# Performance work log

Hardware: AMD Instinct MI355X
Metric: run time of the kernel (lower is better)

The kernel has to match this reference:

```python
import jax, jax.numpy as jnp
import numpy as np

B, T, C = 2, 2048, 2048
N_HEAD, N_KV_HEAD = 16, 4
HEAD_DIM = C // N_HEAD  # 128
HALF = HEAD_DIM // 2    # 64


def _rms_norm(x):
    # F.rms_norm with no weight: x / sqrt(mean(x^2) + eps), eps = dtype eps
    eps = jnp.finfo(x.dtype).eps
    return x * jax.lax.rsqrt(jnp.mean(x * x, axis=-1, keepdims=True) + eps)


def _rope_apply(x, cos, sin):
    # x: [B, H, T, Hs]; cos/sin: [1, 1, T, Hs/2]
    x1, x2 = x[..., :HALF], x[..., HALF:]
    return jnp.concatenate([x1 * cos - x2 * sin, x1 * sin + x2 * cos], axis=-1)


def setup_inputs() -> dict:
    key = jax.random.key(0)
    ks = jax.random.split(key, 8)
    x = jax.random.normal(ks[0], (B, T, C), dtype=jnp.float32)
    # real RoPE tables (base 10000), shape [1,1,T,HALF]
    inv_freq = 1.0 / (10000.0 ** (np.arange(0, HALF, dtype=np.float32) / HALF))
    t = np.arange(T, dtype=np.float32)
    ang = np.einsum('t,f->tf', t, inv_freq)
    cos = jnp.asarray(np.cos(ang))[None, None]
    sin = jnp.asarray(np.sin(ang))[None, None]
    s = 0.02
    Wq = jax.random.normal(ks[1], (C, N_HEAD * HEAD_DIM), dtype=jnp.float32) * s
    Wk = jax.random.normal(ks[2], (C, N_KV_HEAD * HEAD_DIM), dtype=jnp.float32) * s
    Wv = jax.random.normal(ks[3], (C, N_KV_HEAD * HEAD_DIM), dtype=jnp.float32) * s
    Wo = jax.random.normal(ks[4], (C, C), dtype=jnp.float32) * s
    bo = jnp.zeros((C,), dtype=jnp.float32)
    return {"x": x, "cos": cos, "sin": sin, "Wq": Wq, "Wk": Wk, "Wv": Wv, "Wo": Wo, "bo": bo}


def reference(x, cos, sin, Wq, Wk, Wv, Wo, bo):
    Bq, Tq, Cq = x.shape
    G = N_HEAD // N_KV_HEAD
    # QKV projections (GQA, no bias)
    q = (x @ Wq).reshape(Bq, Tq, N_HEAD, HEAD_DIM)
    k = (x @ Wk).reshape(Bq, Tq, N_KV_HEAD, HEAD_DIM)
    v = (x @ Wv).reshape(Bq, Tq, N_KV_HEAD, HEAD_DIM)
    # QK RMSNorm (over head_dim), then to [B, H, T, Hs]
    q = jnp.transpose(_rms_norm(q), (0, 2, 1, 3))
    k = jnp.transpose(_rms_norm(k), (0, 2, 1, 3))
    v = jnp.transpose(v, (0, 2, 1, 3))
    # RoPE
    q = _rope_apply(q, cos[:, :, :Tq, :], sin[:, :, :Tq, :])
    k = _rope_apply(k, cos[:, :, :Tq, :], sin[:, :, :Tq, :])
    # GQA: repeat kv heads across groups
    k = jnp.repeat(k, G, axis=1)  # [B, H, T, Hs]
    v = jnp.repeat(v, G, axis=1)
    # Causal SDPA
    scale = 1.0 / jnp.sqrt(jnp.asarray(HEAD_DIM, dtype=x.dtype))
    scores = jnp.einsum('bhqd,bhkd->bhqk', q, k) * scale
    causal = jnp.tril(jnp.ones((Tq, Tq), dtype=bool))
    scores = jnp.where(causal, scores, jnp.asarray(-jnp.inf, dtype=scores.dtype))
    attn = jax.nn.softmax(scores, axis=-1)
    y = jnp.einsum('bhqk,bhkd->bhqd', attn, v)
    y = jnp.transpose(y, (0, 2, 1, 3)).reshape(Bq, Tq, Cq)
    return y @ Wo + bo
```

## Files before the change

kernel.cpp:

```cpp
#include <hip/hip_runtime.h>
#include <hip/hip_bf16.h>
#include <math.h>

#define BB 2
#define TT 2048
#define CC 2048
#define NH 16
#define NKV 4
#define HD 128
#define HALF 64
#define MTOT (BB*TT)
#define NQKV (CC + 2*NKV*HD)

typedef unsigned short u16;
typedef __attribute__((ext_vector_type(8))) short bf16x8;
typedef __attribute__((ext_vector_type(4))) float f32x4;

__device__ __forceinline__ u16 f2bf(float f) {
  unsigned u = __float_as_uint(f);
  unsigned r = (u + 0x7FFFu + ((u >> 16) & 1u)) >> 16;
  return (u16)r;
}

__device__ __forceinline__ void gl_lds16(const void* g, void* l) {
  __builtin_amdgcn_global_load_lds(
      (const __attribute__((address_space(1))) unsigned int*)g,
      (__attribute__((address_space(3))) unsigned int*)l, 16, 0, 0);
}

__global__ __launch_bounds__(256) void convert_bf16(
    const float* __restrict__ src, u16* __restrict__ dst, int n8) {
  int i = blockIdx.x * 256 + threadIdx.x;
  if (i >= n8) return;
  const float4* s4 = (const float4*)src;
  float4 a = s4[(size_t)i * 2], b = s4[(size_t)i * 2 + 1];
  bf16x8 o;
  o[0] = (short)f2bf(a.x); o[1] = (short)f2bf(a.y);
  o[2] = (short)f2bf(a.z); o[3] = (short)f2bf(a.w);
  o[4] = (short)f2bf(b.x); o[5] = (short)f2bf(b.y);
  o[6] = (short)f2bf(b.z); o[7] = (short)f2bf(b.w);
  ((bf16x8*)dst)[i] = o;
}

__global__ __launch_bounds__(256) void transpose_w(
    const float* __restrict__ W, u16* __restrict__ Wt, int N, int row_off) {
  __shared__ float tile[32][33];
  const int n0 = blockIdx.x * 32, k0 = blockIdx.y * 32;
  const int tx = threadIdx.x, ty = threadIdx.y;
#pragma unroll
  for (int i = 0; i < 4; ++i)
    tile[ty + 8 * i][tx] = W[(size_t)(k0 + ty + 8 * i) * N + n0 + tx];
  __syncthreads();
#pragma unroll
  for (int i = 0; i < 4; ++i)
    Wt[(size_t)(row_off + n0 + ty + 8 * i) * CC + k0 + tx] =
        f2bf(tile[tx][ty + 8 * i]);
}

__global__ __launch_bounds__(256) void v_transpose(
    const float* __restrict__ qkv_lin, u16* __restrict__ vt) {
  __shared__ float tile[32][33];
  const int t0 = blockIdx.x * 32, d0 = blockIdx.y * 32;
  const int p = blockIdx.z;
  const int b = p >> 2, kv = p & 3;
  const int tx = threadIdx.x, ty = threadIdx.y;
#pragma unroll
  for (int i = 0; i < 4; ++i)
    tile[ty + 8 * i][tx] =
        qkv_lin[(size_t)(b * TT + t0 + ty + 8 * i) * NQKV + CC + NKV * HD + kv * HD + d0 + tx];
  __syncthreads();
#pragma unroll
  for (int i = 0; i < 4; ++i)
    vt[((size_t)p * HD + d0 + ty + 8 * i) * TT + t0 + tx] =
        f2bf(tile[tx][ty + 8 * i]);
}

__global__ __launch_bounds__(256) void gemm_bt_bf16(
    const u16* __restrict__ A, const u16* __restrict__ Bt,
    const float* __restrict__ bias, float* __restrict__ C,
    int M, int N, int K) {
  __shared__ u16 As[128 * 32];
  __shared__ u16 Bs[128 * 32];
  const int tid = threadIdx.x;
  const int wave = tid >> 6, lane = tid & 63;
  const int quad = lane >> 4, lo = lane & 15;
  const int bm = blockIdx.y * 128, bn = blockIdx.x * 128;
  const int wm = (wave & 1) * 64, wn = (wave >> 1) * 64;

  f32x4 acc[4][4];
#pragma unroll
  for (int i = 0; i < 4; ++i)
#pragma unroll
    for (int j = 0; j < 4; ++j)
#pragma unroll
      for (int r = 0; r < 4; ++r) acc[i][j][r] = 0.f;

  const int iss0 = wave * 2, iss1 = wave * 2 + 1;
  const int e0 = iss0 * 512 + lane * 8, e1 = iss1 * 512 + lane * 8;
  const int r0 = e0 >> 5, c0 = e0 & 31;
  const int r1 = e1 >> 5, c1 = e1 & 31;

  for (int k0 = 0; k0 < K; k0 += 32) {
    gl_lds16(A + (size_t)(bm + r0) * K + k0 + c0, (char*)As + iss0 * 1024);
    gl_lds16(A + (size_t)(bm + r1) * K + k0 + c1, (char*)As + iss1 * 1024);
    gl_lds16(Bt + (size_t)(bn + r0) * K + k0 + c0, (char*)Bs + iss0 * 1024);
    gl_lds16(Bt + (size_t)(bn + r1) * K + k0 + c1, (char*)Bs + iss1 * 1024);
    __syncthreads();

    bf16x8 af[4], bg[4];
#pragma unroll
    for (int i = 0; i < 4; ++i)
      af[i] = *(const bf16x8*)&As[(wm + i * 16 + lo) * 32 + quad * 8];
#pragma unroll
    for (int j = 0; j < 4; ++j)
      bg[j] = *(const bf16x8*)&Bs[(wn + j * 16 + lo) * 32 + quad * 8];
#pragma unroll
    for (int i = 0; i < 4; ++i)
#pragma unroll
      for (int j = 0; j < 4; ++j)
        acc[i][j] = __builtin_amdgcn_mfma_f32_16x16x32_bf16(af[i], bg[j], acc[i][j], 0, 0, 0);
    __syncthreads();
  }

#pragma unroll
  for (int i = 0; i < 4; ++i)
#pragma unroll
    for (int j = 0; j < 4; ++j)
#pragma unroll
      for (int r = 0; r < 4; ++r) {
        int row = bm + wm + i * 16 + quad * 4 + r;
        int col = bn + wn + j * 16 + lo;
        float v = acc[i][j][r];
        if (bias) v += bias[col];
        C[(size_t)row * N + col] = v;
      }
}

__global__ __launch_bounds__(256) void qkv_post(
    const float* __restrict__ qkv_lin, const float* __restrict__ cosp,
    const float* __restrict__ sinp, u16* __restrict__ q, u16* __restrict__ k) {
  const int bt = blockIdx.x;
  const int hh = blockIdx.y * 4 + (threadIdx.x >> 6);
  const int lane = threadIdx.x & 63;
  const int t = bt & (TT - 1), b = bt >> 11;
  const int col = (hh < NH) ? hh * HD : CC + (hh - NH) * HD;
  const float* src = qkv_lin + (size_t)bt * NQKV + col;
  float v1 = src[lane], v2 = src[lane + 64];
  float ss = v1 * v1 + v2 * v2;
#pragma unroll
  for (int mm = 1; mm < 64; mm <<= 1) ss += __shfl_xor(ss, mm, 64);
  float rms = rsqrtf(ss * (1.f / 128.f) + 1.1920929e-7f);
  float c = cosp[t * HALF + lane], s = sinp[t * HALF + lane];
  float o1 = v1 * rms * c - v2 * rms * s;
  float o2 = v1 * rms * s + v2 * rms * c;
  if (hh < NH) {
    u16* dst = q + (((size_t)(b * NH + hh)) * TT + t) * HD;
    dst[lane] = f2bf(o1); dst[lane + 64] = f2bf(o2);
  } else {
    u16* dst = k + (((size_t)(b * NKV + (hh - NH))) * TT + t) * HD;
    dst[lane] = f2bf(o1); dst[lane + 64] = f2bf(o2);
  }
}

__device__ __forceinline__ void softmax_rb(
    const f32x4* sacc, float* l_lane, u16* Pdst, int rowb, int t0,
    int lo, int quad) {
  const float cc = 0.12751744050808612f;
  if (t0 + 63 > rowb) {
#pragma unroll
    for (int ct = 0; ct < 4; ++ct) {
      const int kvc = ct * 16 + lo;
      const int kcol = t0 + kvc;
      const int idx = (kvc >> 5) * 512 + ((kvc >> 3) & 3) * 128 + quad * 32 + (kvc & 7);
#pragma unroll
      for (int r = 0; r < 4; ++r) {
        float e = __builtin_amdgcn_exp2f(sacc[ct][r] * cc);
        if (kcol > rowb + r) e = 0.f;
        l_lane[r] += e;
        Pdst[idx + r * 8] = f2bf(e);
      }
    }
  } else {
#pragma unroll
    for (int ct = 0; ct < 4; ++ct) {
      const int kvc = ct * 16 + lo;
      const int idx = (kvc >> 5) * 512 + ((kvc >> 3) & 3) * 128 + quad * 32 + (kvc & 7);
#pragma unroll
      for (int r = 0; r < 4; ++r) {
        float e = __builtin_amdgcn_exp2f(sacc[ct][r] * cc);
        l_lane[r] += e;
        Pdst[idx + r * 8] = f2bf(e);
      }
    }
  }
}

__global__ __launch_bounds__(256, 2) void attn_mfma(
    const u16* __restrict__ Qb, const u16* __restrict__ Kb,
    const u16* __restrict__ Vt, u16* __restrict__ Y) {
  __shared__ u16 Ks[2][8192];
  __shared__ u16 Vs[8192];
  __shared__ u16 Ps[4][2048];

  const int qt = blockIdx.x;
  const int bh = blockIdx.y;
  const int b = bh >> 4, h = bh & 15, kvh = h >> 2;
  const int tid = threadIdx.x;
  const int wave = tid >> 6, lane = tid & 63;
  const int quad = lane >> 4, lo = lane & 15;

  const int rowsA = qt * 64;
  const int rowsB = (31 - qt) * 64;
  const u16* Qg = Qb + (size_t)(b * NH + h) * TT * HD;
  const u16* Kg = Kb + (size_t)(b * NKV + kvh) * TT * HD;
  const u16* Vg = Vt + (size_t)(b * NKV + kvh) * HD * TT;

  bf16x8 aq[2][4];
#pragma unroll
  for (int kc = 0; kc < 4; ++kc) {
    aq[0][kc] = *(const bf16x8*)(Qg + (size_t)(rowsA + wave * 16 + lo) * HD + kc * 32 + quad * 8);
    aq[1][kc] = *(const bf16x8*)(Qg + (size_t)(rowsB + wave * 16 + lo) * HD + kc * 32 + quad * 8);
  }

  const u16* kgp[4]; const u16* vgp[4];
  u16* klp[2][4]; u16* vlp[4];
#pragma unroll
  for (int c = 0; c < 4; ++c) {
    const int s = wave * 4 + c;
    const int ct = s >> 2, kq = s & 3;
    kgp[c] = Kg + (size_t)(ct * 16 + lo) * HD + kq * 32 + quad * 8;
    const int dt = s >> 1, k2 = s & 1;
    vgp[c] = Vg + (size_t)(dt * 16 + lo) * TT + k2 * 32 + quad * 8;
    klp[0][c] = &Ks[0][s * 512]; klp[1][c] = &Ks[1][s * 512];
    vlp[c] = &Vs[s * 512];
  }

  f32x4 oacc[2][8];
#pragma unroll
  for (int rb = 0; rb < 2; ++rb)
#pragma unroll
    for (int dt = 0; dt < 8; ++dt)
#pragma unroll
      for (int r = 0; r < 4; ++r) oacc[rb][dt][r] = 0.f;
  float l_lane[2][4];
#pragma unroll
  for (int rb = 0; rb < 2; ++rb)
#pragma unroll
    for (int r = 0; r < 4; ++r) l_lane[rb][r] = 0.f;

  u16* Pw = Ps[wave];
  const int ntiles = 32 - qt;

#pragma unroll
  for (int c = 0; c < 4; ++c) { gl_lds16(kgp[c], klp[0][c]); kgp[c] += 64 * HD; }

  for (int nt = 0; nt < ntiles; ++nt) {
    const int par = nt & 1;
    __syncthreads();
#pragma unroll
    for (int c = 0; c < 4; ++c) { gl_lds16(vgp[c], vlp[c]); vgp[c] += 64; }
    if (nt + 1 < ntiles) {
#pragma unroll
      for (int c = 0; c < 4; ++c) { gl_lds16(kgp[c], klp[par ^ 1][c]); kgp[c] += 64 * HD; }
    }
    const u16* ksb = Ks[par];
    const int t0 = nt * 64;
    const bool act0 = (nt <= qt);

    f32x4 sacc[2][4];
#pragma unroll
    for (int rb = 0; rb < 2; ++rb)
#pragma unroll
      for (int ct = 0; ct < 4; ++ct)
#pragma unroll
        for (int r = 0; r < 4; ++r) sacc[rb][ct][r] = 0.f;
    if (act0) {
#pragma unroll
      for (int ct = 0; ct < 4; ++ct)
#pragma unroll
        for (int kc = 0; kc < 4; ++kc) {
          bf16x8 bk = *(const bf16x8*)&ksb[(ct * 4 + kc) * 512 + lane * 8];
          sacc[0][ct] = __builtin_amdgcn_mfma_f32_16x16x32_bf16(aq[0][kc], bk, sacc[0][ct], 0, 0, 0);
          sacc[1][ct] = __builtin_amdgcn_mfma_f32_16x16x32_bf16(aq[1][kc], bk, sacc[1][ct], 0, 0, 0);
        }
    } else {
#pragma unroll
      for (int ct = 0; ct < 4; ++ct)
#pragma unroll
        for (int kc = 0; kc < 4; ++kc) {
          bf16x8 bk = *(const bf16x8*)&ksb[(ct * 4 + kc) * 512 + lane * 8];
          sacc[1][ct] = __builtin_amdgcn_mfma_f32_16x16x32_bf16(aq[1][kc], bk, sacc[1][ct], 0, 0, 0);
        }
    }

    softmax_rb(sacc[1], l_lane[1], Pw + 1024,
               rowsB + wave * 16 + quad * 4, t0, lo, quad);
    if (act0)
      softmax_rb(sacc[0], l_lane[0], Pw,
                 rowsA + wave * 16 + quad * 4, t0, lo, quad);

    __syncthreads();

    if (act0) {
      bf16x8 ap0[2], ap1[2];
#pragma unroll
      for (int k2 = 0; k2 < 2; ++k2) {
        ap0[k2] = *(const bf16x8*)&Pw[k2 * 512 + lane * 8];
        ap1[k2] = *(const bf16x8*)&Pw[(2 + k2) * 512 + lane * 8];
      }
#pragma unroll
      for (int dt = 0; dt < 8; ++dt)
#pragma unroll
        for (int k2 = 0; k2 < 2; ++k2) {
          bf16x8 bv = *(const bf16x8*)&Vs[(dt * 2 + k2) * 512 + lane * 8];
          oacc[0][dt] = __builtin_amdgcn_mfma_f32_16x16x32_bf16(ap0[k2], bv, oacc[0][dt], 0, 0, 0);
          oacc[1][dt] = __builtin_amdgcn_mfma_f32_16x16x32_bf16(ap1[k2], bv, oacc[1][dt], 0, 0, 0);
        }
    } else {
      bf16x8 ap1[2];
#pragma unroll
      for (int k2 = 0; k2 < 2; ++k2)
        ap1[k2] = *(const bf16x8*)&Pw[(2 + k2) * 512 + lane * 8];
#pragma unroll
      for (int dt = 0; dt < 8; ++dt)
#pragma unroll
        for (int k2 = 0; k2 < 2; ++k2) {
          bf16x8 bv = *(const bf16x8*)&Vs[(dt * 2 + k2) * 512 + lane * 8];
          oacc[1][dt] = __builtin_amdgcn_mfma_f32_16x16x32_bf16(ap1[k2], bv, oacc[1][dt], 0, 0, 0);
        }
    }
  }

#pragma unroll
  for (int rb = 0; rb < 2; ++rb)
#pragma unroll
    for (int r = 0; r < 4; ++r) {
      float l = l_lane[rb][r];
#pragma unroll
      for (int mm = 1; mm < 16; mm <<= 1) l += __shfl_xor(l, mm, 64);
      l_lane[rb][r] = 1.f / l;
    }
#pragma unroll
  for (int rb = 0; rb < 2; ++rb) {
    const int rows = (rb == 0) ? rowsA : rowsB;
    const size_t row0 = (size_t)b * TT + rows + wave * 16 + quad * 4;
#pragma unroll
    for (int dt = 0; dt < 8; ++dt)
#pragma unroll
      for (int r = 0; r < 4; ++r)
        Y[(row0 + r) * CC + h * HD + dt * 16 + lo] = f2bf(oacc[rb][dt][r] * l_lane[rb][r]);
  }
}

extern "C" void kernel_launch(void* const* d_in, const int* in_sizes, int n_in,
                              void* d_out, int out_size, void* d_ws, size_t ws_size,
                              hipStream_t stream) {
  (void)in_sizes; (void)n_in; (void)out_size; (void)ws_size;
  const float* x    = (const float*)d_in[0];
  const float* cosp = (const float*)d_in[1];
  const float* sinp = (const float*)d_in[2];
  const float* Wq   = (const float*)d_in[3];
  const float* Wk   = (const float*)d_in[4];
  const float* Wv   = (const float*)d_in[5];
  const float* Wo   = (const float*)d_in[6];
  const float* bo   = (const float*)d_in[7];
  float* out = (float*)d_out;
  char* ws = (char*)d_ws;

  const size_t MB = 1024 * 1024;
  u16*   xb      = (u16*)(ws);
  u16*   Wt      = (u16*)(ws + 16 * MB);
  float* qkv_lin = (float*)(ws + 28 * MB);
  u16*   Wot     = (u16*)(ws + 76 * MB);
  u16*   qb_buf  = (u16*)(ws);
  u16*   kb      = (u16*)(ws + 16 * MB);
  u16*   vt      = (u16*)(ws + 20 * MB);
  u16*   y       = (u16*)(ws + 28 * MB);

  convert_bf16<<<(MTOT * CC / 8 + 255) / 256, 256, 0, stream>>>(x, xb, MTOT * CC / 8);

  transpose_w<<<dim3(CC / 32, CC / 32), dim3(32, 8), 0, stream>>>(Wq, Wt, CC, 0);
  transpose_w<<<dim3(NKV * HD / 32, CC / 32), dim3(32, 8), 0, stream>>>(Wk, Wt, NKV * HD, CC);
  transpose_w<<<dim3(NKV * HD / 32, CC / 32), dim3(32, 8), 0, stream>>>(Wv, Wt, NKV * HD, CC + NKV * HD);
  transpose_w<<<dim3(CC / 32, CC / 32), dim3(32, 8), 0, stream>>>(Wo, Wot, CC, 0);

  gemm_bt_bf16<<<dim3(NQKV / 128, MTOT / 128), 256, 0, stream>>>(
      xb, Wt, nullptr, qkv_lin, MTOT, NQKV, CC);

  qkv_post<<<dim3(MTOT, 5), 256, 0, stream>>>(qkv_lin, cosp, sinp, qb_buf, kb);

  v_transpose<<<dim3(TT / 32, HD / 32, BB * NKV), dim3(32, 8), 0, stream>>>(qkv_lin, vt);

  attn_mfma<<<dim3(16, BB * NH), 256, 0, stream>>>(qb_buf, kb, vt, y);

  gemm_bt_bf16<<<dim3(CC / 128, MTOT / 128), 256, 0, stream>>>(
      y, Wot, bo, out, MTOT, CC, CC);
}
```

Measured before the change: 345.4 us.

## Fuse prep kernels, emit bf16 QKV, keep attention P in registers

Merges the x conversion and the four weight transposes into one launch. The QKV GEMM now writes bf16 instead of fp32, which halves that intermediate's traffic for qkv_post and v_transpose. In attention, S is computed transposed so the softmax probabilities can be packed straight into MFMA operand registers. This removes the P round-trip through LDS and one barrier per tile, and V is double-buffered with its prefetch moved alongside K. V's transpose is permuted to match the new register layout, and the extra bf16 rounding of the QKV intermediate adds a small precision cost.

```diff
diff --git a/kernel.cpp b/kernel.cpp
--- a/kernel.cpp
+++ b/kernel.cpp
@@ -21,6 +21,9 @@
   unsigned r = (u + 0x7FFFu + ((u >> 16) & 1u)) >> 16;
   return (u16)r;
 }
+__device__ __forceinline__ float bf2f(u16 v) {
+  return __uint_as_float(((unsigned)v) << 16);
+}
 
 __device__ __forceinline__ void gl_lds16(const void* g, void* l) {
   __builtin_amdgcn_global_load_lds(
@@ -28,57 +31,48 @@
       (__attribute__((address_space(3))) unsigned int*)l, 16, 0, 0);
 }
 
-__global__ __launch_bounds__(256) void convert_bf16(
-    const float* __restrict__ src, u16* __restrict__ dst, int n8) {
-  int i = blockIdx.x * 256 + threadIdx.x;
-  if (i >= n8) return;
-  const float4* s4 = (const float4*)src;
-  float4 a = s4[(size_t)i * 2], b = s4[(size_t)i * 2 + 1];
-  bf16x8 o;
-  o[0] = (short)f2bf(a.x); o[1] = (short)f2bf(a.y);
-  o[2] = (short)f2bf(a.z); o[3] = (short)f2bf(a.w);
-  o[4] = (short)f2bf(b.x); o[5] = (short)f2bf(b.y);
-  o[6] = (short)f2bf(b.z); o[7] = (short)f2bf(b.w);
-  ((bf16x8*)dst)[i] = o;
-}
-
-__global__ __launch_bounds__(256) void transpose_w(
-    const float* __restrict__ W, u16* __restrict__ Wt, int N, int row_off) {
+__global__ __launch_bounds__(256) void prep(
+    const float* __restrict__ x, const float* __restrict__ Wq,
+    const float* __restrict__ Wk, const float* __restrict__ Wv,
+    const float* __restrict__ Wo, u16* __restrict__ xb,
+    u16* __restrict__ Wt, u16* __restrict__ Wot) {
+  const int z = blockIdx.z;
+  const int tx = threadIdx.x, ty = threadIdx.y;
+  if (z == 4) {
+    const int tid = ty * 32 + tx;
+    const int i = (blockIdx.y * 64 + blockIdx.x) * 256 + tid;
+    const float4* s4 = (const float4*)x;
+    float4 a = s4[(size_t)i * 2], b = s4[(size_t)i * 2 + 1];
+    bf16x8 o;
+    o[0] = (short)f2bf(a.x); o[1] = (short)f2bf(a.y);
+    o[2] = (short)f2bf(a.z); o[3] = (short)f2bf(a.w);
+    o[4] = (short)f2bf(b.x); o[5] = (short)f2bf(b.y);
+    o[6] = (short)f2bf(b.z); o[7] = (short)f2bf(b.w);
+    ((bf16x8*)xb)[i] = o;
+    return;
+  }
+  const float* W; u16* dst; int N; int row_off;
+  if (z == 0)      { W = Wq; dst = Wt;  N = 2048; row_off = 0; }
+  else if (z == 1) { W = Wk; dst = Wt;  N = 512;  row_off = 2048; }
+  else if (z == 2) { W = Wv; dst = Wt;  N = 512;  row_off = 2560; }
+  else             { W = Wo; dst = Wot; N = 2048; row_off = 0; }
+  const int n0 = blockIdx.x * 32, k0 = blockIdx.y * 32;
+  if (n0 >= N) return;
   __shared__ float tile[32][33];
-  const int n0 = blockIdx.x * 32, k0 = blockIdx.y * 32;
-  const int tx = threadIdx.x, ty = threadIdx.y;
 #pragma unroll
   for (int i = 0; i < 4; ++i)
     tile[ty + 8 * i][tx] = W[(size_t)(k0 + ty + 8 * i) * N + n0 + tx];
   __syncthreads();
 #pragma unroll
   for (int i = 0; i < 4; ++i)
-    Wt[(size_t)(row_off + n0 + ty + 8 * i) * CC + k0 + tx] =
-        f2bf(tile[tx][ty + 8 * i]);
-}
-
-__global__ __launch_bounds__(256) void v_transpose(
-    const float* __restrict__ qkv_lin, u16* __restrict__ vt) {
-  __shared__ float tile[32][33];
-  const int t0 = blockIdx.x * 32, d0 = blockIdx.y * 32;
-  const int p = blockIdx.z;
-  const int b = p >> 2, kv = p & 3;
-  const int tx = threadIdx.x, ty = threadIdx.y;
-#pragma unroll
-  for (int i = 0; i < 4; ++i)
-    tile[ty + 8 * i][tx] =
-        qkv_lin[(size_t)(b * TT + t0 + ty + 8 * i) * NQKV + CC + NKV * HD + kv * HD + d0 + tx];
-  __syncthreads();
-#pragma unroll
-  for (int i = 0; i < 4; ++i)
-    vt[((size_t)p * HD + d0 + ty + 8 * i) * TT + t0 + tx] =
+    dst[(size_t)(row_off + n0 + ty + 8 * i) * CC + k0 + tx] =
         f2bf(tile[tx][ty + 8 * i]);
 }
 
 __global__ __launch_bounds__(256) void gemm_bt_bf16(
     const u16* __restrict__ A, const u16* __restrict__ Bt,
     const float* __restrict__ bias, float* __restrict__ C,
-    int M, int N, int K) {
+    int M, int N, int K, int out_bf16) {
   __shared__ u16 As[128 * 32];
   __shared__ u16 Bs[128 * 32];
   const int tid = threadIdx.x;
@@ -132,20 +126,21 @@
         int col = bn + wn + j * 16 + lo;
         float v = acc[i][j][r];
         if (bias) v += bias[col];
-        C[(size_t)row * N + col] = v;
+        if (out_bf16) ((u16*)C)[(size_t)row * N + col] = f2bf(v);
+        else          C[(size_t)row * N + col] = v;
       }
 }
 
 __global__ __launch_bounds__(256) void qkv_post(
-    const float* __restrict__ qkv_lin, const float* __restrict__ cosp,
+    const u16* __restrict__ qkv_lin, const float* __restrict__ cosp,
     const float* __restrict__ sinp, u16* __restrict__ q, u16* __restrict__ k) {
   const int bt = blockIdx.x;
   const int hh = blockIdx.y * 4 + (threadIdx.x >> 6);
   const int lane = threadIdx.x & 63;
   const int t = bt & (TT - 1), b = bt >> 11;
   const int col = (hh < NH) ? hh * HD : CC + (hh - NH) * HD;
-  const float* src = qkv_lin + (size_t)bt * NQKV + col;
-  float v1 = src[lane], v2 = src[lane + 64];
+  const u16* src = qkv_lin + (size_t)bt * NQKV + col;
+  float v1 = bf2f(src[lane]), v2 = bf2f(src[lane + 64]);
   float ss = v1 * v1 + v2 * v2;
 #pragma unroll
   for (int mm = 1; mm < 64; mm <<= 1) ss += __shfl_xor(ss, mm, 64);
@@ -162,36 +157,54 @@
   }
 }
 
-__device__ __forceinline__ void softmax_rb(
-    const f32x4* sacc, float* l_lane, u16* Pdst, int rowb, int t0,
-    int lo, int quad) {
+__global__ __launch_bounds__(256) void v_transpose(
+    const u16* __restrict__ qkv_lin, u16* __restrict__ vt) {
+  __shared__ u16 tile[32][33];
+  const int t0 = blockIdx.x * 32, d0 = blockIdx.y * 32;
+  const int p = blockIdx.z;
+  const int b = p >> 2, kv = p & 3;
+  const int tx = threadIdx.x, ty = threadIdx.y;
+#pragma unroll
+  for (int i = 0; i < 4; ++i)
+    tile[ty + 8 * i][tx] =
+        qkv_lin[(size_t)(b * TT + t0 + ty + 8 * i) * NQKV + CC + NKV * HD + kv * HD + d0 + tx];
+  __syncthreads();
+  const int tperm = ((tx >> 2) & 3) * 8 + (tx & 3) + 4 * ((tx >> 4) & 1);
+#pragma unroll
+  for (int i = 0; i < 4; ++i)
+    vt[((size_t)p * HD + d0 + ty + 8 * i) * TT + t0 + tperm] = tile[tx][ty + 8 * i];
+}
+
+__device__ __forceinline__ void softmax_pack(
+    const f32x4* sacc, float& l_lane, bf16x8* ap, int rowq, int t0,
+    bool diag, int quad) {
   const float cc = 0.12751744050808612f;
-  if (t0 + 63 > rowb) {
-#pragma unroll
-    for (int ct = 0; ct < 4; ++ct) {
-      const int kvc = ct * 16 + lo;
-      const int kcol = t0 + kvc;
-      const int idx = (kvc >> 5) * 512 + ((kvc >> 3) & 3) * 128 + quad * 32 + (kvc & 7);
+  float e[4][4];
+  if (diag) {
+#pragma unroll
+    for (int ct = 0; ct < 4; ++ct)
 #pragma unroll
       for (int r = 0; r < 4; ++r) {
-        float e = __builtin_amdgcn_exp2f(sacc[ct][r] * cc);
-        if (kcol > rowb + r) e = 0.f;
-        l_lane[r] += e;
-        Pdst[idx + r * 8] = f2bf(e);
-      }
-    }
+        float v = __builtin_amdgcn_exp2f(sacc[ct][r] * cc);
+        if (t0 + ct * 16 + quad * 4 + r > rowq) v = 0.f;
+        l_lane += v; e[ct][r] = v;
+      }
   } else {
 #pragma unroll
-    for (int ct = 0; ct < 4; ++ct) {
-      const int kvc = ct * 16 + lo;
-      const int idx = (kvc >> 5) * 512 + ((kvc >> 3) & 3) * 128 + quad * 32 + (kvc & 7);
+    for (int ct = 0; ct < 4; ++ct)
 #pragma unroll
       for (int r = 0; r < 4; ++r) {
-        float e = __builtin_amdgcn_exp2f(sacc[ct][r] * cc);
-        l_lane[r] += e;
-        Pdst[idx + r * 8] = f2bf(e);
-      }
-    }
+        float v = __builtin_amdgcn_exp2f(sacc[ct][r] * cc);
+        l_lane += v; e[ct][r] = v;
+      }
+  }
+#pragma unroll
+  for (int k2 = 0; k2 < 2; ++k2) {
+    bf16x8 ch;
+#pragma unroll
+    for (int j = 0; j < 8; ++j)
+      ch[j] = (short)f2bf(e[k2 * 2 + (j >> 2)][j & 3]);
+    ap[k2] = ch;
   }
 }
 
@@ -199,8 +212,7 @@
     const u16* __restrict__ Qb, const u16* __restrict__ Kb,
     const u16* __restrict__ Vt, u16* __restrict__ Y) {
   __shared__ u16 Ks[2][8192];
-  __shared__ u16 Vs[8192];
-  __shared__ u16 Ps[4][2048];
+  __shared__ u16 Vs[2][8192];
 
   const int qt = blockIdx.x;
   const int bh = blockIdx.y;
@@ -209,8 +221,7 @@
   const int wave = tid >> 6, lane = tid & 63;
   const int quad = lane >> 4, lo = lane & 15;
 
-  const int rowsA = qt * 64;
-  const int rowsB = (31 - qt) * 64;
+  const int rowsA = qt * 64, rowsB = (31 - qt) * 64;
   const u16* Qg = Qb + (size_t)(b * NH + h) * TT * HD;
   const u16* Kg = Kb + (size_t)(b * NKV + kvh) * TT * HD;
   const u16* Vg = Vt + (size_t)(b * NKV + kvh) * HD * TT;
@@ -223,7 +234,7 @@
   }
 
   const u16* kgp[4]; const u16* vgp[4];
-  u16* klp[2][4]; u16* vlp[4];
+  u16* klp[2][4]; u16* vlp[2][4];
 #pragma unroll
   for (int c = 0; c < 4; ++c) {
     const int s = wave * 4 + c;
@@ -232,7 +243,7 @@
     const int dt = s >> 1, k2 = s & 1;
     vgp[c] = Vg + (size_t)(dt * 16 + lo) * TT + k2 * 32 + quad * 8;
     klp[0][c] = &Ks[0][s * 512]; klp[1][c] = &Ks[1][s * 512];
-    vlp[c] = &Vs[s * 512];
+    vlp[0][c] = &Vs[0][s * 512]; vlp[1][c] = &Vs[1][s * 512];
   }
 
   f32x4 oacc[2][8];
@@ -242,28 +253,30 @@
     for (int dt = 0; dt < 8; ++dt)
 #pragma unroll
       for (int r = 0; r < 4; ++r) oacc[rb][dt][r] = 0.f;
-  float l_lane[2][4];
-#pragma unroll
-  for (int rb = 0; rb < 2; ++rb)
-#pragma unroll
-    for (int r = 0; r < 4; ++r) l_lane[rb][r] = 0.f;
-
-  u16* Pw = Ps[wave];
+  float l_lane[2] = {0.f, 0.f};
+
   const int ntiles = 32 - qt;
-
-#pragma unroll
-  for (int c = 0; c < 4; ++c) { gl_lds16(kgp[c], klp[0][c]); kgp[c] += 64 * HD; }
+  const int rowqA = rowsA + wave * 16 + lo;
+  const int rowqB = rowsB + wave * 16 + lo;
+
+#pragma unroll
+  for (int c = 0; c < 4; ++c) {
+    gl_lds16(kgp[c], klp[0][c]); kgp[c] += 64 * HD;
+    gl_lds16(vgp[c], vlp[0][c]); vgp[c] += 64;
+  }
 
   for (int nt = 0; nt < ntiles; ++nt) {
     const int par = nt & 1;
     __syncthreads();
-#pragma unroll
-    for (int c = 0; c < 4; ++c) { gl_lds16(vgp[c], vlp[c]); vgp[c] += 64; }
     if (nt + 1 < ntiles) {
 #pragma unroll
-      for (int c = 0; c < 4; ++c) { gl_lds16(kgp[c], klp[par ^ 1][c]); kgp[c] += 64 * HD; }
+      for (int c = 0; c < 4; ++c) {
+        gl_lds16(kgp[c], klp[par ^ 1][c]); kgp[c] += 64 * HD;
+        gl_lds16(vgp[c], vlp[par ^ 1][c]); vgp[c] += 64;
+      }
     }
     const u16* ksb = Ks[par];
+    const u16* vsb = Vs[par];
     const int t0 = nt * 64;
     const bool act0 = (nt <= qt);
 
@@ -274,72 +287,45 @@
       for (int ct = 0; ct < 4; ++ct)
 #pragma unroll
         for (int r = 0; r < 4; ++r) sacc[rb][ct][r] = 0.f;
-    if (act0) {
-#pragma unroll
-      for (int ct = 0; ct < 4; ++ct)
-#pragma unroll
-        for (int kc = 0; kc < 4; ++kc) {
-          bf16x8 bk = *(const bf16x8*)&ksb[(ct * 4 + kc) * 512 + lane * 8];
-          sacc[0][ct] = __builtin_amdgcn_mfma_f32_16x16x32_bf16(aq[0][kc], bk, sacc[0][ct], 0, 0, 0);
-          sacc[1][ct] = __builtin_amdgcn_mfma_f32_16x16x32_bf16(aq[1][kc], bk, sacc[1][ct], 0, 0, 0);
-        }
-    } else {
-#pragma unroll
-      for (int ct = 0; ct < 4; ++ct)
-#pragma unroll
-        for (int kc = 0; kc < 4; ++kc) {
-          bf16x8 bk = *(const bf16x8*)&ksb[(ct * 4 + kc) * 512 + lane * 8];
-          sacc[1][ct] = __builtin_amdgcn_mfma_f32_16x16x32_bf16(aq[1][kc], bk, sacc[1][ct], 0, 0, 0);
-        }
-    }
-
-    softmax_rb(sacc[1], l_lane[1], Pw + 1024,
-               rowsB + wave * 16 + quad * 4, t0, lo, quad);
+#pragma unroll
+    for (int ct = 0; ct < 4; ++ct)
+#pragma unroll
+      for (int kc = 0; kc < 4; ++kc) {
+        bf16x8 bk = *(const bf16x8*)&ksb[(ct * 4 + kc) * 512 + lane * 8];
+        sacc[1][ct] = __builtin_amdgcn_mfma_f32_16x16x32_bf16(bk, aq[1][kc], sacc[1][ct], 0, 0, 0);
+        if (act0)
+          sacc[0][ct] = __builtin_amdgcn_mfma_f32_16x16x32_bf16(bk, aq[0][kc], sacc[0][ct], 0, 0, 0);
+      }
+
+    bf16x8 ap[2][2];
+    softmax_pack(sacc[1], l_lane[1], ap[1], rowqB, t0,
+                 t0 + 63 > rowsB + wave * 16, quad);
     if (act0)
-      softmax_rb(sacc[0], l_lane[0], Pw,
-                 rowsA + wave * 16 + quad * 4, t0, lo, quad);
-
-    __syncthreads();
-
-    if (act0) {
-      bf16x8 ap0[2], ap1[2];
+      softmax_pack(sacc[0], l_lane[0], ap[0], rowqA, t0,
+                   t0 + 63 > rowsA + wave * 16, quad);
+
+#pragma unroll
+    for (int dt = 0; dt < 8; ++dt)
 #pragma unroll
       for (int k2 = 0; k2 < 2; ++k2) {
-        ap0[k2] = *(const bf16x8*)&Pw[k2 * 512 + lane * 8];
-        ap1[k2] = *(const bf16x8*)&Pw[(2 + k2) * 512 + lane * 8];
-      }
-#pragma unroll
-      for (int dt = 0; dt < 8; ++dt)
-#pragma unroll
-        for (int k2 = 0; k2 < 2; ++k2) {
-          bf16x8 bv = *(const bf16x8*)&Vs[(dt * 2 + k2) * 512 + lane * 8];
-          oacc[0][dt] = __builtin_amdgcn_mfma_f32_16x16x32_bf16(ap0[k2], bv, oacc[0][dt], 0, 0, 0);
-          oacc[1][dt] = __builtin_amdgcn_mfma_f32_16x16x32_bf16(ap1[k2], bv, oacc[1][dt], 0, 0, 0);
-        }
-    } else {
-      bf16x8 ap1[2];
-#pragma unroll
-      for (int k2 = 0; k2 < 2; ++k2)
-        ap1[k2] = *(const bf16x8*)&Pw[(2 + k2) * 512 + lane * 8];
-#pragma unroll
-      for (int dt = 0; dt < 8; ++dt)
-#pragma unroll
-        for (int k2 = 0; k2 < 2; ++k2) {
-          bf16x8 bv = *(const bf16x8*)&Vs[(dt * 2 + k2) * 512 + lane * 8];
-          oacc[1][dt] = __builtin_amdgcn_mfma_f32_16x16x32_bf16(ap1[k2], bv, oacc[1][dt], 0, 0, 0);
-        }
-    }
-  }
-
-#pragma unroll
-  for (int rb = 0; rb < 2; ++rb)
-#pragma unroll
-    for (int r = 0; r < 4; ++r) {
-      float l = l_lane[rb][r];
-#pragma unroll
-      for (int mm = 1; mm < 16; mm <<= 1) l += __shfl_xor(l, mm, 64);
-      l_lane[rb][r] = 1.f / l;
-    }
+        bf16x8 bv = *(const bf16x8*)&vsb[(dt * 2 + k2) * 512 + lane * 8];
+        oacc[1][dt] = __builtin_amdgcn_mfma_f32_16x16x32_bf16(ap[1][k2], bv, oacc[1][dt], 0, 0, 0);
+        if (act0)
+          oacc[0][dt] = __builtin_amdgcn_mfma_f32_16x16x32_bf16(ap[0][k2], bv, oacc[0][dt], 0, 0, 0);
+      }
+  }
+
+  float linv[2][4];
+#pragma unroll
+  for (int rb = 0; rb < 2; ++rb) {
+    float l = l_lane[rb];
+    l += __shfl_xor(l, 16, 64);
+    l += __shfl_xor(l, 32, 64);
+    l = 1.f / l;
+#pragma unroll
+    for (int r = 0; r < 4; ++r)
+      linv[rb][r] = __shfl(l, quad * 4 + r, 64);
+  }
 #pragma unroll
   for (int rb = 0; rb < 2; ++rb) {
     const int rows = (rb == 0) ? rowsA : rowsB;
@@ -348,7 +334,7 @@
     for (int dt = 0; dt < 8; ++dt)
 #pragma unroll
       for (int r = 0; r < 4; ++r)
-        Y[(row0 + r) * CC + h * HD + dt * 16 + lo] = f2bf(oacc[rb][dt][r] * l_lane[rb][r]);
+        Y[(row0 + r) * CC + h * HD + dt * 16 + lo] = f2bf(oacc[rb][dt][r] * linv[rb][r]);
   }
 }
 
@@ -368,24 +354,19 @@
   char* ws = (char*)d_ws;
 
   const size_t MB = 1024 * 1024;
-  u16*   xb      = (u16*)(ws);
-  u16*   Wt      = (u16*)(ws + 16 * MB);
-  float* qkv_lin = (float*)(ws + 28 * MB);
-  u16*   Wot     = (u16*)(ws + 76 * MB);
-  u16*   qb_buf  = (u16*)(ws);
-  u16*   kb      = (u16*)(ws + 16 * MB);
-  u16*   vt      = (u16*)(ws + 20 * MB);
-  u16*   y       = (u16*)(ws + 28 * MB);
-
-  convert_bf16<<<(MTOT * CC / 8 + 255) / 256, 256, 0, stream>>>(x, xb, MTOT * CC / 8);
-
-  transpose_w<<<dim3(CC / 32, CC / 32), dim3(32, 8), 0, stream>>>(Wq, Wt, CC, 0);
-  transpose_w<<<dim3(NKV * HD / 32, CC / 32), dim3(32, 8), 0, stream>>>(Wk, Wt, NKV * HD, CC);
-  transpose_w<<<dim3(NKV * HD / 32, CC / 32), dim3(32, 8), 0, stream>>>(Wv, Wt, NKV * HD, CC + NKV * HD);
-  transpose_w<<<dim3(CC / 32, CC / 32), dim3(32, 8), 0, stream>>>(Wo, Wot, CC, 0);
+  u16* xb      = (u16*)(ws);
+  u16* Wt      = (u16*)(ws + 16 * MB);
+  u16* qkv_lin = (u16*)(ws + 28 * MB);
+  u16* Wot     = (u16*)(ws + 52 * MB);
+  u16* qb_buf  = (u16*)(ws);
+  u16* kb      = (u16*)(ws + 16 * MB);
+  u16* vt      = (u16*)(ws + 20 * MB);
+  u16* y       = (u16*)(ws + 28 * MB);
+
+  prep<<<dim3(64, 64, 5), dim3(32, 8), 0, stream>>>(x, Wq, Wk, Wv, Wo, xb, Wt, Wot);
 
   gemm_bt_bf16<<<dim3(NQKV / 128, MTOT / 128), 256, 0, stream>>>(
-      xb, Wt, nullptr, qkv_lin, MTOT, NQKV, CC);
+      xb, Wt, nullptr, (float*)qkv_lin, MTOT, NQKV, CC, 1);
 
   qkv_post<<<dim3(MTOT, 5), 256, 0, stream>>>(qkv_lin, cosp, sinp, qb_buf, kb);
 
@@ -394,5 +375,5 @@
   attn_mfma<<<dim3(16, BB * NH), 256, 0, stream>>>(qb_buf, kb, vt, y);
 
   gemm_bt_bf16<<<dim3(CC / 128, MTOT / 128), 256, 0, stream>>>(
-      y, Wot, bo, out, MTOT, CC, CC);
-}
+      y, Wot, bo, out, MTOT, CC, CC, 0);
+}
```

After: 336.7 us. 1.03x faster.
